# Kernel tuning notes

Measured on AMD Instinct MI355X. Metric: run time of the kernel, lower is better.

The kernel has to match this reference:

```python
import jax, jax.numpy as jnp
import numpy as np
import math

IN_DIM = 256
OUT_DIM = 256
MAX_IN = 1024
MAX_OUT = 512
BATCH = 2
SEQ = 1024  # actual_seq_len == max_in_seq here
RED = 2
LN_EPS = 1e-5


def setup_inputs() -> dict:
    key = jax.random.key(0)
    ks = jax.random.split(key, 8)
    N = BATCH * SEQ
    return {
        "x": jax.random.normal(ks[0], (N, IN_DIM), dtype=jnp.float32),
        "M": jax.random.uniform(ks[1], (OUT_DIM, IN_DIM), minval=-0.5, maxval=0.5, dtype=jnp.float32),
        "P": jax.random.uniform(ks[2], (OUT_DIM, OUT_DIM), minval=-0.1, maxval=0.1, dtype=jnp.float32),
        "Linker": jax.random.uniform(ks[3], (MAX_IN, MAX_OUT), minval=-0.1, maxval=0.1, dtype=jnp.float32),
        "ln_gamma": jnp.ones((OUT_DIM,), dtype=jnp.float32),
        "ln_beta": jnp.zeros((OUT_DIM,), dtype=jnp.float32),
        "res_W": jax.random.uniform(ks[4], (OUT_DIM, IN_DIM), minval=-0.1, maxval=0.1, dtype=jnp.float32),
        "res_linker": jax.random.uniform(ks[5], (MAX_IN, MAX_OUT), minval=-0.1, maxval=0.1, dtype=jnp.float32),
        "actual_seq_len": SEQ,
    }


def _layer_norm(z, gamma, beta):
    mu = jnp.mean(z, axis=-1, keepdims=True)
    var = jnp.mean((z - mu) ** 2, axis=-1, keepdims=True)
    return (z - mu) * jax.lax.rsqrt(var + LN_EPS) * gamma + beta


def _periods():
    i = jnp.arange(OUT_DIM, dtype=jnp.float32)[:, None]
    j = jnp.arange(OUT_DIM, dtype=jnp.float32)[None, :]
    return i * OUT_DIM + j + 2.0  # (D, D)


def reference(x, M, P, Linker, ln_gamma, ln_beta, res_W, res_linker, actual_seq_len):
    S = int(actual_seq_len)
    N, _ = x.shape
    B = N // S
    D = OUT_DIM
    out_seq = max(1, S // RED)

    # Z = LN(x @ M^T)
    Z = _layer_norm(x @ M.T, ln_gamma, ln_beta)  # (N, D)

    # position transform: T[k,i] = sum_j Z[k,j] * P[i,j] * cos(2*pi*k / periods[i,j])
    k = jnp.arange(N, dtype=jnp.float32)[:, None, None]  # (N,1,1)
    phi = jnp.cos(2.0 * math.pi * k / _periods()[None])   # (N, D, D)
    T = jnp.einsum('kj,ij,kij->ki', Z, P, phi)            # (N, D)

    # adaptive sequence-length transform via Linker slice
    L = Linker[:S, :out_seq]                               # (S, out_seq)
    U = jnp.einsum('bsd,st->btd', T.reshape(B, S, D), L).reshape(B * out_seq, D)

    # 'separate' residual path
    rfeat = (x @ res_W.T).reshape(B, S, D)
    rL = res_linker[:S, :out_seq]
    residual = jnp.einsum('bsd,st->btd', rfeat, rL).reshape(B * out_seq, D)

    return U + residual
```

## Files before the change

### kernel.cpp

```cpp
#include <hip/hip_runtime.h>

#define D256 256
#define KT 8
#define S_SEQ 1024
#define OUTSEQ 512

typedef __attribute__((ext_vector_type(8))) short bf16x8;
typedef __attribute__((ext_vector_type(8))) unsigned short u16x8;
typedef __attribute__((ext_vector_type(4))) unsigned short u16x4;
typedef __attribute__((ext_vector_type(4))) float f32x4;

__device__ inline unsigned short f2bf(float f) {
  unsigned u = __float_as_uint(f);
  return (unsigned short)((u + 0x7fffu + ((u >> 16) & 1u)) >> 16);
}

__global__ __launch_bounds__(256) void k_prep(const float* __restrict__ x,
                                              const float* __restrict__ M,
                                              const float* __restrict__ resW,
                                              const float* __restrict__ P,
                                              const float* __restrict__ Linker,
                                              const float* __restrict__ rLinker,
                                              float4* __restrict__ PIt4,
                                              unsigned short* __restrict__ LinkTb,
                                              unsigned short* __restrict__ xb,
                                              unsigned short* __restrict__ Mb,
                                              unsigned short* __restrict__ Wb) {
  __shared__ float tl[64][65];
  const int tid = threadIdx.x;
  const int blk = blockIdx.x;
  if (blk < 256) {
    const int j = blk;
    const int t = tid;
    const float p = (float)(t * D256 + j + 2);
    const float ip = 1.0f / p;
    const float cb2 = 2.0f * __builtin_amdgcn_cosf(ip);
    PIt4[j * D256 + t] = make_float4(P[t * D256 + j], ip, cb2, 0.0f);
    return;
  }
  if (blk >= 512) {
    const float* src;
    unsigned short* dst;
    size_t base;
    if (blk < 768)      { src = x;    dst = xb; base = (size_t)(blk - 512) * 2048; }
    else if (blk < 800) { src = M;    dst = Mb; base = (size_t)(blk - 768) * 2048; }
    else                { src = resW; dst = Wb; base = (size_t)(blk - 800) * 2048; }
    const size_t off = base + (size_t)tid * 8;
    const float4 v0 = *(const float4*)(src + off);
    const float4 v1 = *(const float4*)(src + off + 4);
    u16x8 o;
    o[0] = f2bf(v0.x); o[1] = f2bf(v0.y); o[2] = f2bf(v0.z); o[3] = f2bf(v0.w);
    o[4] = f2bf(v1.x); o[5] = f2bf(v1.y); o[6] = f2bf(v1.z); o[7] = f2bf(v1.w);
    *(u16x8*)(dst + off) = o;
    return;
  }
  const int tb = blk - 256;
  const int st = tb & 31;
  const int tt = tb >> 5;
  const int s0 = st * 64, t0 = tt * 64;
  const float* src = (s0 < 1024) ? (Linker + (size_t)s0 * OUTSEQ)
                                 : (rLinker + (size_t)(s0 - 1024) * OUTSEQ);
  {
    const int sy = tid >> 2, sx = tid & 3;
    #pragma unroll
    for (int c = 0; c < 4; ++c) {
      const int ci = sx + c * 4;
      const float4 v = *(const float4*)&src[sy * OUTSEQ + t0 + ci * 4];
      tl[ci * 4 + 0][sy] = v.x;
      tl[ci * 4 + 1][sy] = v.y;
      tl[ci * 4 + 2][sy] = v.z;
      tl[ci * 4 + 3][sy] = v.w;
    }
  }
  __syncthreads();
  {
    const int ty = tid >> 2, tx = tid & 3;
    u16x8 o0, o1;
    #pragma unroll
    for (int e = 0; e < 8; ++e) o0[e] = f2bf(tl[ty][tx * 16 + e]);
    #pragma unroll
    for (int e = 0; e < 8; ++e) o1[e] = f2bf(tl[ty][tx * 16 + 8 + e]);
    unsigned short* dst = LinkTb + (size_t)(t0 + ty) * 2048 + s0 + tx * 16;
    *(u16x8*)dst = o0;
    *(u16x8*)(dst + 8) = o1;
  }
}

__global__ __launch_bounds__(256) void k_Azn(const unsigned short* __restrict__ xb,
                                             const unsigned short* __restrict__ Mb,
                                             const unsigned short* __restrict__ Wb,
                                             const float* __restrict__ gamma,
                                             const float* __restrict__ beta,
                                             float* __restrict__ Zb,
                                             unsigned short* __restrict__ Bt) {
  __shared__ float Zs[16][D256];
  __shared__ float Rs[16][D256];
  __shared__ float mu_s[16], rs_s[16];
  const int k0 = blockIdx.x * 16;
  const int w = threadIdx.x >> 6;
  const int l = threadIdx.x & 63;
  const int m = l & 15, q = l >> 4;

  f32x4 aZ[4] = {}, aR[4] = {};
  const unsigned short* Arow = xb + (size_t)(k0 + m) * D256;
  #pragma unroll
  for (int ks = 0; ks < 8; ++ks) {
    const bf16x8 a = *(const bf16x8*)(Arow + ks * 32 + q * 8);
    #pragma unroll
    for (int cf = 0; cf < 4; ++cf) {
      const int o = w * 64 + cf * 16 + m;
      const bf16x8 bz = *(const bf16x8*)(Mb + (size_t)o * D256 + ks * 32 + q * 8);
      const bf16x8 br = *(const bf16x8*)(Wb + (size_t)o * D256 + ks * 32 + q * 8);
      aZ[cf] = __builtin_amdgcn_mfma_f32_16x16x32_bf16(a, bz, aZ[cf], 0, 0, 0);
      aR[cf] = __builtin_amdgcn_mfma_f32_16x16x32_bf16(a, br, aR[cf], 0, 0, 0);
    }
  }
  #pragma unroll
  for (int cf = 0; cf < 4; ++cf) {
    #pragma unroll
    for (int r = 0; r < 4; ++r) {
      Zs[q * 4 + r][w * 64 + cf * 16 + m] = aZ[cf][r];
      Rs[q * 4 + r][w * 64 + cf * 16 + m] = aR[cf][r];
    }
  }
  __syncthreads();

  #pragma unroll
  for (int rr = w; rr < 16; rr += 4) {
    float s = 0.f, sq = 0.f;
    #pragma unroll
    for (int p = 0; p < 4; ++p) {
      const float v = Zs[rr][l + 64 * p];
      s += v;
      sq = fmaf(v, v, sq);
    }
    #pragma unroll
    for (int off = 32; off; off >>= 1) {
      s += __shfl_down(s, off);
      sq += __shfl_down(sq, off);
    }
    if (l == 0) {
      const float mu = s * (1.0f / 256.0f);
      const float var = sq * (1.0f / 256.0f) - mu * mu;
      mu_s[rr] = mu;
      rs_s[rr] = rsqrtf(var + 1e-5f);
    }
  }
  __syncthreads();

  {
    const int t = threadIdx.x;
    const float g = gamma[t], be = beta[t];
    u16x8 o0, o1;
    #pragma unroll
    for (int rr = 0; rr < 16; ++rr) {
      Zb[(size_t)(k0 + rr) * D256 + t] = (Zs[rr][t] - mu_s[rr]) * rs_s[rr] * g + be;
      const unsigned short rb = f2bf(Rs[rr][t]);
      if (rr < 8) o0[rr] = rb; else o1[rr - 8] = rb;
    }
    unsigned short* dst = Bt + (size_t)t * 4096 + 2048 + k0;
    *(u16x8*)dst = o0;
    *(u16x8*)(dst + 8) = o1;
  }
}

__global__ __launch_bounds__(256, 6) void k_B(const float* __restrict__ Zb,
                                              const float4* __restrict__ PIt4,
                                              unsigned short* __restrict__ Bt) {
  __shared__ float buf[5120];
  const int tid = threadIdx.x;
  const int il = tid & 7;
  const int jg = tid >> 3;
  const int ig = blockIdx.x & 31;
  const int kt = blockIdx.x >> 5;
  const int i0 = ig * 8;
  const int k0 = kt * 16;
  const int i  = i0 + il;

  #pragma unroll
  for (int r = 0; r < 16; ++r)
    buf[tid * 20 + r] = Zb[(size_t)(k0 + r) * D256 + tid];
  __syncthreads();

  float acc[16] = {};
  const float kf0 = (float)k0;
  const float4* pip = PIt4 + i;
  #pragma unroll
  for (int jj = 0; jj < 8; ++jj) {
    const int j = jg + 32 * jj;
    const float4 pi = pip[(size_t)j * D256];
    const float4 z0 = *(const float4*)&buf[j * 20 + 0];
    const float4 z1 = *(const float4*)&buf[j * 20 + 4];
    const float4 z2 = *(const float4*)&buf[j * 20 + 8];
    const float4 z3 = *(const float4*)&buf[j * 20 + 12];
    const float a = kf0 * pi.y;
    float c0 = __builtin_amdgcn_cosf(__builtin_amdgcn_fractf(a)) * pi.x;
    float c1 = __builtin_amdgcn_cosf(__builtin_amdgcn_fractf(a + pi.y)) * pi.x;
    acc[0] = fmaf(z0.x, c0, acc[0]);
    acc[1] = fmaf(z0.y, c1, acc[1]);
    float c2;
    c2 = fmaf(pi.z, c1, -c0); acc[2]  = fmaf(z0.z, c2, acc[2]);  c0 = c1; c1 = c2;
    c2 = fmaf(pi.z, c1, -c0); acc[3]  = fmaf(z0.w, c2, acc[3]);  c0 = c1; c1 = c2;
    c2 = fmaf(pi.z, c1, -c0); acc[4]  = fmaf(z1.x, c2, acc[4]);  c0 = c1; c1 = c2;
    c2 = fmaf(pi.z, c1, -c0); acc[5]  = fmaf(z1.y, c2, acc[5]);  c0 = c1; c1 = c2;
    c2 = fmaf(pi.z, c1, -c0); acc[6]  = fmaf(z1.z, c2, acc[6]);  c0 = c1; c1 = c2;
    c2 = fmaf(pi.z, c1, -c0); acc[7]  = fmaf(z1.w, c2, acc[7]);  c0 = c1; c1 = c2;
    c2 = fmaf(pi.z, c1, -c0); acc[8]  = fmaf(z2.x, c2, acc[8]);  c0 = c1; c1 = c2;
    c2 = fmaf(pi.z, c1, -c0); acc[9]  = fmaf(z2.y, c2, acc[9]);  c0 = c1; c1 = c2;
    c2 = fmaf(pi.z, c1, -c0); acc[10] = fmaf(z2.z, c2, acc[10]); c0 = c1; c1 = c2;
    c2 = fmaf(pi.z, c1, -c0); acc[11] = fmaf(z2.w, c2, acc[11]); c0 = c1; c1 = c2;
    c2 = fmaf(pi.z, c1, -c0); acc[12] = fmaf(z3.x, c2, acc[12]); c0 = c1; c1 = c2;
    c2 = fmaf(pi.z, c1, -c0); acc[13] = fmaf(z3.y, c2, acc[13]); c0 = c1; c1 = c2;
    c2 = fmaf(pi.z, c1, -c0); acc[14] = fmaf(z3.z, c2, acc[14]); c0 = c1; c1 = c2;
    c2 = fmaf(pi.z, c1, -c0); acc[15] = fmaf(z3.w, c2, acc[15]);
  }
  __syncthreads();

  #pragma unroll
  for (int k = 0; k < 16; ++k)
    buf[jg * 132 + k * 8 + il] = acc[k];
  __syncthreads();

  float tv = 0.f;
  if (tid < 128) {
    #pragma unroll
    for (int g = 0; g < 32; ++g) tv += buf[g * 132 + tid];
  }
  __syncthreads();
  if (tid < 128) buf[(tid & 7) * 16 + (tid >> 3)] = tv;
  __syncthreads();
  if (tid < 32) {
    const int iw = tid >> 2;
    const int kq = tid & 3;
    const float4 v = *(const float4*)&buf[iw * 16 + kq * 4];
    u16x4 o;
    o[0] = f2bf(v.x); o[1] = f2bf(v.y); o[2] = f2bf(v.z); o[3] = f2bf(v.w);
    *(u16x4*)(Bt + (size_t)(i0 + iw) * 4096 + k0 + kq * 4) = o;
  }
}

__global__ __launch_bounds__(256) void k_Cm(const unsigned short* __restrict__ LinkTb,
                                            const unsigned short* __restrict__ Bt,
                                            float* __restrict__ part) {
  const int bid = blockIdx.x;
  const int kc = bid & 7;
  const int dt = (bid >> 3) & 3;
  const int tt = (bid >> 5) & 7;
  const int b  = bid >> 8;
  const int wv = threadIdx.x >> 6;
  const int l  = threadIdx.x & 63;
  const int wm = wv >> 1, wn = wv & 1;
  const int t0 = tt * 64 + wm * 32;
  const int d0 = dt * 64 + wn * 32;
  const int m  = l & 15;
  const int q  = l >> 4;
  const int sc0 = kc * 128;

  f32x4 acc00 = {}, acc01 = {}, acc10 = {}, acc11 = {};
  const unsigned short* Arow = LinkTb + (size_t)(t0 + m) * 2048;
  const unsigned short* Brow = Bt + (size_t)(d0 + m) * 4096;

  #pragma unroll
  for (int seg = 0; seg < 2; ++seg) {
    const int acol = seg * 1024 + sc0 + q * 8;
    const int bcol = seg * 2048 + b * 1024 + sc0 + q * 8;
    #pragma unroll
    for (int ks = 0; ks < 4; ++ks) {
      const bf16x8 a0 = *(const bf16x8*)(Arow + acol + ks * 32);
      const bf16x8 a1 = *(const bf16x8*)(Arow + 16 * 2048 + acol + ks * 32);
      const bf16x8 b0 = *(const bf16x8*)(Brow + bcol + ks * 32);
      const bf16x8 b1 = *(const bf16x8*)(Brow + 16 * 4096 + bcol + ks * 32);
      acc00 = __builtin_amdgcn_mfma_f32_16x16x32_bf16(a0, b0, acc00, 0, 0, 0);
      acc01 = __builtin_amdgcn_mfma_f32_16x16x32_bf16(a0, b1, acc01, 0, 0, 0);
      acc10 = __builtin_amdgcn_mfma_f32_16x16x32_bf16(a1, b0, acc10, 0, 0, 0);
      acc11 = __builtin_amdgcn_mfma_f32_16x16x32_bf16(a1, b1, acc11, 0, 0, 0);
    }
  }

  float* pb = part + ((size_t)kc << 18) + (size_t)(b * 512 + t0 + q * 4) * D256 + d0 + m;
  #pragma unroll
  for (int reg = 0; reg < 4; ++reg) {
    pb[(0 + reg) * D256 + 0]   = acc00[reg];
    pb[(0 + reg) * D256 + 16]  = acc01[reg];
    pb[(16 + reg) * D256 + 0]  = acc10[reg];
    pb[(16 + reg) * D256 + 16] = acc11[reg];
  }
}

__global__ __launch_bounds__(256) void k_Cred(const float* __restrict__ part,
                                              float* __restrict__ out) {
  const int row = blockIdx.x;
  const int d   = threadIdx.x;
  float s = 0.f;
  #pragma unroll
  for (int kc = 0; kc < 8; ++kc)
    s += part[((size_t)kc << 18) + row * D256 + d];
  out[row * D256 + d] = s;
}

extern "C" void kernel_launch(void* const* d_in, const int* in_sizes, int n_in,
                              void* d_out, int out_size, void* d_ws, size_t ws_size,
                              hipStream_t stream) {
  const float* x       = (const float*)d_in[0];
  const float* M       = (const float*)d_in[1];
  const float* P       = (const float*)d_in[2];
  const float* Linker  = (const float*)d_in[3];
  const float* gamma   = (const float*)d_in[4];
  const float* beta    = (const float*)d_in[5];
  const float* resW    = (const float*)d_in[6];
  const float* rLinker = (const float*)d_in[7];
  float* out = (float*)d_out;

  char* ws = (char*)d_ws;
  float4*         PIt4   = (float4*)(ws);
  unsigned short* LinkTb = (unsigned short*)(ws + 1024 * 1024);
  unsigned short* Bt     = (unsigned short*)(ws + 3072 * 1024);
  unsigned short* xb     = (unsigned short*)(ws + 5120 * 1024);
  unsigned short* Mb     = (unsigned short*)(ws + 6144 * 1024);
  unsigned short* Wb     = (unsigned short*)(ws + 6272 * 1024);
  float*          Zb     = (float*)(ws + 6400 * 1024);
  float*          part   = (float*)(ws + 8448 * 1024);

  hipLaunchKernelGGL(k_prep, dim3(832),  dim3(256), 0, stream,
                     x, M, resW, P, Linker, rLinker, PIt4, LinkTb, xb, Mb, Wb);
  hipLaunchKernelGGL(k_Azn,  dim3(128),  dim3(256), 0, stream,
                     xb, Mb, Wb, gamma, beta, Zb, Bt);
  hipLaunchKernelGGL(k_B,    dim3(4096), dim3(256), 0, stream, Zb, PIt4, Bt);
  hipLaunchKernelGGL(k_Cm,   dim3(512),  dim3(256), 0, stream, LinkTb, Bt, part);
  hipLaunchKernelGGL(k_Cred, dim3(1024), dim3(256), 0, stream, part, out);
}
```

Measured before the change: 49.77 us.

## Fuse prep with projection+LayerNorm and reduce split-K partials in shared memory

The first projection GEMM plus LayerNorm now loads fp32 inputs directly and converts them to bf16 in registers. It is merged into the prep kernel, which removes the separate bf16 conversion pass and one launch. The final linker GEMM splits K across the four waves of a block and reduces their partials in LDS. This replaces the global partial buffer and the separate reduction kernel. The change cuts two launches and the partial-sum traffic, at the cost of redundant fp32 loads and conversions of M/resW in each projection block and fewer blocks (256) in the final GEMM.

```diff
diff --git a/kernel.cpp b/kernel.cpp
--- a/kernel.cpp
+++ b/kernel.cpp
@@ -15,22 +15,109 @@
   return (unsigned short)((u + 0x7fffu + ((u >> 16) & 1u)) >> 16);
 }
 
-__global__ __launch_bounds__(256) void k_prep(const float* __restrict__ x,
-                                              const float* __restrict__ M,
-                                              const float* __restrict__ resW,
-                                              const float* __restrict__ P,
-                                              const float* __restrict__ Linker,
-                                              const float* __restrict__ rLinker,
-                                              float4* __restrict__ PIt4,
-                                              unsigned short* __restrict__ LinkTb,
-                                              unsigned short* __restrict__ xb,
-                                              unsigned short* __restrict__ Mb,
-                                              unsigned short* __restrict__ Wb) {
-  __shared__ float tl[64][65];
+__device__ inline bf16x8 ld8bf(const float* p) {
+  const float4 v0 = *(const float4*)p;
+  const float4 v1 = *(const float4*)(p + 4);
+  bf16x8 r;
+  r[0] = (short)f2bf(v0.x); r[1] = (short)f2bf(v0.y);
+  r[2] = (short)f2bf(v0.z); r[3] = (short)f2bf(v0.w);
+  r[4] = (short)f2bf(v1.x); r[5] = (short)f2bf(v1.y);
+  r[6] = (short)f2bf(v1.z); r[7] = (short)f2bf(v1.w);
+  return r;
+}
+
+__global__ __launch_bounds__(256) void k_pre(const float* __restrict__ x,
+                                             const float* __restrict__ M,
+                                             const float* __restrict__ resW,
+                                             const float* __restrict__ P,
+                                             const float* __restrict__ Linker,
+                                             const float* __restrict__ rLinker,
+                                             const float* __restrict__ gamma,
+                                             const float* __restrict__ beta,
+                                             float4* __restrict__ PIt4,
+                                             unsigned short* __restrict__ LinkTb,
+                                             float* __restrict__ Zb,
+                                             unsigned short* __restrict__ Bt) {
+  __shared__ float smem[8224];
   const int tid = threadIdx.x;
   const int blk = blockIdx.x;
-  if (blk < 256) {
-    const int j = blk;
+
+  if (blk < 128) {
+    float (*Zs)[D256] = (float(*)[D256])smem;
+    float (*Rs)[D256] = (float(*)[D256])(smem + 4096);
+    float* mu_s = smem + 8192;
+    float* rs_s = smem + 8208;
+    const int k0 = blk * 16;
+    const int w = tid >> 6;
+    const int l = tid & 63;
+    const int m = l & 15, q = l >> 4;
+
+    f32x4 aZ[4] = {}, aR[4] = {};
+    const float* xrow = x + (size_t)(k0 + m) * D256;
+    #pragma unroll
+    for (int ks = 0; ks < 8; ++ks) {
+      const bf16x8 a = ld8bf(xrow + ks * 32 + q * 8);
+      #pragma unroll
+      for (int cf = 0; cf < 4; ++cf) {
+        const int o = w * 64 + cf * 16 + m;
+        const bf16x8 bz = ld8bf(M    + (size_t)o * D256 + ks * 32 + q * 8);
+        const bf16x8 br = ld8bf(resW + (size_t)o * D256 + ks * 32 + q * 8);
+        aZ[cf] = __builtin_amdgcn_mfma_f32_16x16x32_bf16(a, bz, aZ[cf], 0, 0, 0);
+        aR[cf] = __builtin_amdgcn_mfma_f32_16x16x32_bf16(a, br, aR[cf], 0, 0, 0);
+      }
+    }
+    #pragma unroll
+    for (int cf = 0; cf < 4; ++cf) {
+      #pragma unroll
+      for (int r = 0; r < 4; ++r) {
+        Zs[q * 4 + r][w * 64 + cf * 16 + m] = aZ[cf][r];
+        Rs[q * 4 + r][w * 64 + cf * 16 + m] = aR[cf][r];
+      }
+    }
+    __syncthreads();
+
+    #pragma unroll
+    for (int rr = w; rr < 16; rr += 4) {
+      float s = 0.f, sq = 0.f;
+      #pragma unroll
+      for (int p = 0; p < 4; ++p) {
+        const float v = Zs[rr][l + 64 * p];
+        s += v;
+        sq = fmaf(v, v, sq);
+      }
+      #pragma unroll
+      for (int off = 32; off; off >>= 1) {
+        s += __shfl_down(s, off);
+        sq += __shfl_down(sq, off);
+      }
+      if (l == 0) {
+        const float mu = s * (1.0f / 256.0f);
+        const float var = sq * (1.0f / 256.0f) - mu * mu;
+        mu_s[rr] = mu;
+        rs_s[rr] = rsqrtf(var + 1e-5f);
+      }
+    }
+    __syncthreads();
+
+    {
+      const int t = tid;
+      const float g = gamma[t], be = beta[t];
+      u16x8 o0, o1;
+      #pragma unroll
+      for (int rr = 0; rr < 16; ++rr) {
+        Zb[(size_t)(k0 + rr) * D256 + t] = (Zs[rr][t] - mu_s[rr]) * rs_s[rr] * g + be;
+        const unsigned short rb = f2bf(Rs[rr][t]);
+        if (rr < 8) o0[rr] = rb; else o1[rr - 8] = rb;
+      }
+      unsigned short* dst = Bt + (size_t)t * 4096 + 2048 + k0;
+      *(u16x8*)dst = o0;
+      *(u16x8*)(dst + 8) = o1;
+    }
+    return;
+  }
+
+  if (blk < 384) {
+    const int j = blk - 128;
     const int t = tid;
     const float p = (float)(t * D256 + j + 2);
     const float ip = 1.0f / p;
@@ -38,23 +125,9 @@
     PIt4[j * D256 + t] = make_float4(P[t * D256 + j], ip, cb2, 0.0f);
     return;
   }
-  if (blk >= 512) {
-    const float* src;
-    unsigned short* dst;
-    size_t base;
-    if (blk < 768)      { src = x;    dst = xb; base = (size_t)(blk - 512) * 2048; }
-    else if (blk < 800) { src = M;    dst = Mb; base = (size_t)(blk - 768) * 2048; }
-    else                { src = resW; dst = Wb; base = (size_t)(blk - 800) * 2048; }
-    const size_t off = base + (size_t)tid * 8;
-    const float4 v0 = *(const float4*)(src + off);
-    const float4 v1 = *(const float4*)(src + off + 4);
-    u16x8 o;
-    o[0] = f2bf(v0.x); o[1] = f2bf(v0.y); o[2] = f2bf(v0.z); o[3] = f2bf(v0.w);
-    o[4] = f2bf(v1.x); o[5] = f2bf(v1.y); o[6] = f2bf(v1.z); o[7] = f2bf(v1.w);
-    *(u16x8*)(dst + off) = o;
-    return;
-  }
-  const int tb = blk - 256;
+
+  float (*tl)[65] = (float(*)[65])smem;
+  const int tb = blk - 384;
   const int st = tb & 31;
   const int tt = tb >> 5;
   const int s0 = st * 64, t0 = tt * 64;
@@ -81,84 +154,6 @@
     #pragma unroll
     for (int e = 0; e < 8; ++e) o1[e] = f2bf(tl[ty][tx * 16 + 8 + e]);
     unsigned short* dst = LinkTb + (size_t)(t0 + ty) * 2048 + s0 + tx * 16;
-    *(u16x8*)dst = o0;
-    *(u16x8*)(dst + 8) = o1;
-  }
-}
-
-__global__ __launch_bounds__(256) void k_Azn(const unsigned short* __restrict__ xb,
-                                             const unsigned short* __restrict__ Mb,
-                                             const unsigned short* __restrict__ Wb,
-                                             const float* __restrict__ gamma,
-                                             const float* __restrict__ beta,
-                                             float* __restrict__ Zb,
-                                             unsigned short* __restrict__ Bt) {
-  __shared__ float Zs[16][D256];
-  __shared__ float Rs[16][D256];
-  __shared__ float mu_s[16], rs_s[16];
-  const int k0 = blockIdx.x * 16;
-  const int w = threadIdx.x >> 6;
-  const int l = threadIdx.x & 63;
-  const int m = l & 15, q = l >> 4;
-
-  f32x4 aZ[4] = {}, aR[4] = {};
-  const unsigned short* Arow = xb + (size_t)(k0 + m) * D256;
-  #pragma unroll
-  for (int ks = 0; ks < 8; ++ks) {
-    const bf16x8 a = *(const bf16x8*)(Arow + ks * 32 + q * 8);
-    #pragma unroll
-    for (int cf = 0; cf < 4; ++cf) {
-      const int o = w * 64 + cf * 16 + m;
-      const bf16x8 bz = *(const bf16x8*)(Mb + (size_t)o * D256 + ks * 32 + q * 8);
-      const bf16x8 br = *(const bf16x8*)(Wb + (size_t)o * D256 + ks * 32 + q * 8);
-      aZ[cf] = __builtin_amdgcn_mfma_f32_16x16x32_bf16(a, bz, aZ[cf], 0, 0, 0);
-      aR[cf] = __builtin_amdgcn_mfma_f32_16x16x32_bf16(a, br, aR[cf], 0, 0, 0);
-    }
-  }
-  #pragma unroll
-  for (int cf = 0; cf < 4; ++cf) {
-    #pragma unroll
-    for (int r = 0; r < 4; ++r) {
-      Zs[q * 4 + r][w * 64 + cf * 16 + m] = aZ[cf][r];
-      Rs[q * 4 + r][w * 64 + cf * 16 + m] = aR[cf][r];
-    }
-  }
-  __syncthreads();
-
-  #pragma unroll
-  for (int rr = w; rr < 16; rr += 4) {
-    float s = 0.f, sq = 0.f;
-    #pragma unroll
-    for (int p = 0; p < 4; ++p) {
-      const float v = Zs[rr][l + 64 * p];
-      s += v;
-      sq = fmaf(v, v, sq);
-    }
-    #pragma unroll
-    for (int off = 32; off; off >>= 1) {
-      s += __shfl_down(s, off);
-      sq += __shfl_down(sq, off);
-    }
-    if (l == 0) {
-      const float mu = s * (1.0f / 256.0f);
-      const float var = sq * (1.0f / 256.0f) - mu * mu;
-      mu_s[rr] = mu;
-      rs_s[rr] = rsqrtf(var + 1e-5f);
-    }
-  }
-  __syncthreads();
-
-  {
-    const int t = threadIdx.x;
-    const float g = gamma[t], be = beta[t];
-    u16x8 o0, o1;
-    #pragma unroll
-    for (int rr = 0; rr < 16; ++rr) {
-      Zb[(size_t)(k0 + rr) * D256 + t] = (Zs[rr][t] - mu_s[rr]) * rs_s[rr] * g + be;
-      const unsigned short rb = f2bf(Rs[rr][t]);
-      if (rr < 8) o0[rr] = rb; else o1[rr - 8] = rb;
-    }
-    unsigned short* dst = Bt + (size_t)t * 4096 + 2048 + k0;
     *(u16x8*)dst = o0;
     *(u16x8*)(dst + 8) = o1;
   }
@@ -241,20 +236,18 @@
 
 __global__ __launch_bounds__(256) void k_Cm(const unsigned short* __restrict__ LinkTb,
                                             const unsigned short* __restrict__ Bt,
-                                            float* __restrict__ part) {
+                                            float* __restrict__ out) {
+  __shared__ float red[4][32][32];
   const int bid = blockIdx.x;
-  const int kc = bid & 7;
-  const int dt = (bid >> 3) & 3;
-  const int tt = (bid >> 5) & 7;
-  const int b  = bid >> 8;
-  const int wv = threadIdx.x >> 6;
+  const int ct = bid & 7;
+  const int rt = bid >> 3;
+  const int b  = rt >> 4;
+  const int t0 = (rt & 15) * 32;
+  const int d0 = ct * 32;
+  const int w  = threadIdx.x >> 6;
   const int l  = threadIdx.x & 63;
-  const int wm = wv >> 1, wn = wv & 1;
-  const int t0 = tt * 64 + wm * 32;
-  const int d0 = dt * 64 + wn * 32;
-  const int m  = l & 15;
-  const int q  = l >> 4;
-  const int sc0 = kc * 128;
+  const int m  = l & 15, q = l >> 4;
+  const int s0 = w * 256;
 
   f32x4 acc00 = {}, acc01 = {}, acc10 = {}, acc11 = {};
   const unsigned short* Arow = LinkTb + (size_t)(t0 + m) * 2048;
@@ -262,10 +255,10 @@
 
   #pragma unroll
   for (int seg = 0; seg < 2; ++seg) {
-    const int acol = seg * 1024 + sc0 + q * 8;
-    const int bcol = seg * 2048 + b * 1024 + sc0 + q * 8;
-    #pragma unroll
-    for (int ks = 0; ks < 4; ++ks) {
+    const int acol = seg * 1024 + s0 + q * 8;
+    const int bcol = seg * 2048 + b * 1024 + s0 + q * 8;
+    #pragma unroll
+    for (int ks = 0; ks < 8; ++ks) {
       const bf16x8 a0 = *(const bf16x8*)(Arow + acol + ks * 32);
       const bf16x8 a1 = *(const bf16x8*)(Arow + 16 * 2048 + acol + ks * 32);
       const bf16x8 b0 = *(const bf16x8*)(Brow + bcol + ks * 32);
@@ -277,25 +270,27 @@
     }
   }
 
-  float* pb = part + ((size_t)kc << 18) + (size_t)(b * 512 + t0 + q * 4) * D256 + d0 + m;
-  #pragma unroll
-  for (int reg = 0; reg < 4; ++reg) {
-    pb[(0 + reg) * D256 + 0]   = acc00[reg];
-    pb[(0 + reg) * D256 + 16]  = acc01[reg];
-    pb[(16 + reg) * D256 + 0]  = acc10[reg];
-    pb[(16 + reg) * D256 + 16] = acc11[reg];
-  }
-}
-
-__global__ __launch_bounds__(256) void k_Cred(const float* __restrict__ part,
-                                              float* __restrict__ out) {
-  const int row = blockIdx.x;
-  const int d   = threadIdx.x;
-  float s = 0.f;
-  #pragma unroll
-  for (int kc = 0; kc < 8; ++kc)
-    s += part[((size_t)kc << 18) + row * D256 + d];
-  out[row * D256 + d] = s;
+  #pragma unroll
+  for (int r = 0; r < 4; ++r) {
+    red[w][q * 4 + r][m]           = acc00[r];
+    red[w][q * 4 + r][16 + m]      = acc01[r];
+    red[w][16 + q * 4 + r][m]      = acc10[r];
+    red[w][16 + q * 4 + r][16 + m] = acc11[r];
+  }
+  __syncthreads();
+
+  const int row = threadIdx.x >> 3;
+  const int c4  = (threadIdx.x & 7) * 4;
+  const float4 v0 = *(const float4*)&red[0][row][c4];
+  const float4 v1 = *(const float4*)&red[1][row][c4];
+  const float4 v2 = *(const float4*)&red[2][row][c4];
+  const float4 v3 = *(const float4*)&red[3][row][c4];
+  float4 s;
+  s.x = v0.x + v1.x + v2.x + v3.x;
+  s.y = v0.y + v1.y + v2.y + v3.y;
+  s.z = v0.z + v1.z + v2.z + v3.z;
+  s.w = v0.w + v1.w + v2.w + v3.w;
+  *(float4*)&out[(size_t)(b * 512 + t0 + row) * D256 + d0 + c4] = s;
 }
 
 extern "C" void kernel_launch(void* const* d_in, const int* in_sizes, int n_in,
@@ -315,17 +310,11 @@
   float4*         PIt4   = (float4*)(ws);
   unsigned short* LinkTb = (unsigned short*)(ws + 1024 * 1024);
   unsigned short* Bt     = (unsigned short*)(ws + 3072 * 1024);
-  unsigned short* xb     = (unsigned short*)(ws + 5120 * 1024);
-  unsigned short* Mb     = (unsigned short*)(ws + 6144 * 1024);
-  unsigned short* Wb     = (unsigned short*)(ws + 6272 * 1024);
-  float*          Zb     = (float*)(ws + 6400 * 1024);
-  float*          part   = (float*)(ws + 8448 * 1024);
-
-  hipLaunchKernelGGL(k_prep, dim3(832),  dim3(256), 0, stream,
-                     x, M, resW, P, Linker, rLinker, PIt4, LinkTb, xb, Mb, Wb);
-  hipLaunchKernelGGL(k_Azn,  dim3(128),  dim3(256), 0, stream,
-                     xb, Mb, Wb, gamma, beta, Zb, Bt);
-  hipLaunchKernelGGL(k_B,    dim3(4096), dim3(256), 0, stream, Zb, PIt4, Bt);
-  hipLaunchKernelGGL(k_Cm,   dim3(512),  dim3(256), 0, stream, LinkTb, Bt, part);
-  hipLaunchKernelGGL(k_Cred, dim3(1024), dim3(256), 0, stream, part, out);
-}
+  float*          Zb     = (float*)(ws + 5120 * 1024);
+
+  hipLaunchKernelGGL(k_pre, dim3(640),  dim3(256), 0, stream,
+                     x, M, resW, P, Linker, rLinker, gamma, beta,
+                     PIt4, LinkTb, Zb, Bt);
+  hipLaunchKernelGGL(k_B,   dim3(4096), dim3(256), 0, stream, Zb, PIt4, Bt);
+  hipLaunchKernelGGL(k_Cm,  dim3(256),  dim3(256), 0, stream, LinkTb, Bt, out);
+}
```

Result: slower. 51.07 us (+2.6%).

## Restructure position-transform kernel with stride-2 packed cosine recurrence and transposed Z

Applied to the files above, without the earlier changes.

The LN output Z is now written transposed (feature-major), so k_B can read each feature's 32 consecutive sequence values straight from global memory instead of staging them in LDS. k_B now covers 32 positions per block and steps the Chebyshev cosine recurrence by two. It uses a precomputed 4cos²θ−2 coefficient and packed f32x2 FMAs, which roughly halves the FMA instruction count. The cross-thread reduction is simplified to a single LDS pass with scalar bf16 stores. The trade-offs are more register pressure (occupancy hint lowered from 6 to 4), a larger LDS buffer, and uncoalesced 2-byte output stores.

```diff
diff --git a/kernel.cpp b/kernel.cpp
--- a/kernel.cpp
+++ b/kernel.cpp
@@ -1,14 +1,13 @@
 #include <hip/hip_runtime.h>
 
 #define D256 256
-#define KT 8
 #define S_SEQ 1024
 #define OUTSEQ 512
 
 typedef __attribute__((ext_vector_type(8))) short bf16x8;
 typedef __attribute__((ext_vector_type(8))) unsigned short u16x8;
-typedef __attribute__((ext_vector_type(4))) unsigned short u16x4;
 typedef __attribute__((ext_vector_type(4))) float f32x4;
+typedef __attribute__((ext_vector_type(2))) float f32x2;
 
 __device__ inline unsigned short f2bf(float f) {
   unsigned u = __float_as_uint(f);
@@ -35,7 +34,8 @@
     const float p = (float)(t * D256 + j + 2);
     const float ip = 1.0f / p;
     const float cb2 = 2.0f * __builtin_amdgcn_cosf(ip);
-    PIt4[j * D256 + t] = make_float4(P[t * D256 + j], ip, cb2, 0.0f);
+    const float D = fmaf(cb2, cb2, -2.0f);
+    PIt4[j * D256 + t] = make_float4(P[t * D256 + j], ip, cb2, D);
     return;
   }
   if (blk >= 512) {
@@ -91,7 +91,7 @@
                                              const unsigned short* __restrict__ Wb,
                                              const float* __restrict__ gamma,
                                              const float* __restrict__ beta,
-                                             float* __restrict__ Zb,
+                                             float* __restrict__ ZbT,
                                              unsigned short* __restrict__ Bt) {
   __shared__ float Zs[16][D256];
   __shared__ float Rs[16][D256];
@@ -151,92 +151,102 @@
   {
     const int t = threadIdx.x;
     const float g = gamma[t], be = beta[t];
+    float zt[16];
     u16x8 o0, o1;
     #pragma unroll
     for (int rr = 0; rr < 16; ++rr) {
-      Zb[(size_t)(k0 + rr) * D256 + t] = (Zs[rr][t] - mu_s[rr]) * rs_s[rr] * g + be;
+      zt[rr] = (Zs[rr][t] - mu_s[rr]) * rs_s[rr] * g + be;
       const unsigned short rb = f2bf(Rs[rr][t]);
       if (rr < 8) o0[rr] = rb; else o1[rr - 8] = rb;
     }
+    float* zd = ZbT + (size_t)t * 2048 + k0;
+    *(float4*)(zd + 0)  = make_float4(zt[0], zt[1], zt[2], zt[3]);
+    *(float4*)(zd + 4)  = make_float4(zt[4], zt[5], zt[6], zt[7]);
+    *(float4*)(zd + 8)  = make_float4(zt[8], zt[9], zt[10], zt[11]);
+    *(float4*)(zd + 12) = make_float4(zt[12], zt[13], zt[14], zt[15]);
     unsigned short* dst = Bt + (size_t)t * 4096 + 2048 + k0;
     *(u16x8*)dst = o0;
     *(u16x8*)(dst + 8) = o1;
   }
 }
 
-__global__ __launch_bounds__(256, 6) void k_B(const float* __restrict__ Zb,
+__global__ __launch_bounds__(256, 4) void k_B(const float* __restrict__ ZbT,
                                               const float4* __restrict__ PIt4,
                                               unsigned short* __restrict__ Bt) {
-  __shared__ float buf[5120];
+  __shared__ float buf[8448];
   const int tid = threadIdx.x;
   const int il = tid & 7;
   const int jg = tid >> 3;
   const int ig = blockIdx.x & 31;
   const int kt = blockIdx.x >> 5;
   const int i0 = ig * 8;
-  const int k0 = kt * 16;
+  const int k0 = kt * 32;
   const int i  = i0 + il;
 
-  #pragma unroll
-  for (int r = 0; r < 16; ++r)
-    buf[tid * 20 + r] = Zb[(size_t)(k0 + r) * D256 + tid];
+  f32x2 acc[16];
+  #pragma unroll
+  for (int q = 0; q < 16; ++q) acc[q] = (f32x2){0.f, 0.f};
+
+  const float kf0 = (float)k0;
+  #pragma unroll
+  for (int jj = 0; jj < 8; ++jj) {
+    const int j = jg * 8 + jj;
+    const f32x4 pi = *(const f32x4*)&PIt4[(size_t)j * D256 + i];
+    const float* zr = ZbT + (size_t)j * 2048 + k0;
+    const f32x4 z0 = *(const f32x4*)(zr + 0);
+    const f32x4 z1 = *(const f32x4*)(zr + 4);
+    const f32x4 z2 = *(const f32x4*)(zr + 8);
+    const f32x4 z3 = *(const f32x4*)(zr + 12);
+    const f32x4 z4 = *(const f32x4*)(zr + 16);
+    const f32x4 z5 = *(const f32x4*)(zr + 20);
+    const f32x4 z6 = *(const f32x4*)(zr + 24);
+    const f32x4 z7 = *(const f32x4*)(zr + 28);
+    const float a  = kf0 * pi.y;
+    const float r0 = __builtin_amdgcn_fractf(a);
+    const float r1 = __builtin_amdgcn_fractf(a + pi.y);
+    const float s0 = __builtin_amdgcn_cosf(r0) * pi.x;
+    const float s1 = __builtin_amdgcn_cosf(r1) * pi.x;
+    const float s2 = fmaf(pi.z, s1, -s0);
+    const float s3 = fmaf(pi.z, s2, -s1);
+    f32x2 pm1 = {s0, s1};
+    f32x2 pm  = {s2, s3};
+    const f32x2 D2 = {pi.w, pi.w};
+    acc[0] = __builtin_elementwise_fma((f32x2){z0.x, z0.y}, pm1, acc[0]);
+    acc[1] = __builtin_elementwise_fma((f32x2){z0.z, z0.w}, pm,  acc[1]);
+    f32x2 pn;
+#define CSTEP(IDX, ZA, ZB) \
+    pn = __builtin_elementwise_fma(D2, pm, -pm1); \
+    acc[IDX] = __builtin_elementwise_fma((f32x2){ZA, ZB}, pn, acc[IDX]); \
+    pm1 = pm; pm = pn;
+    CSTEP(2,  z1.x, z1.y)
+    CSTEP(3,  z1.z, z1.w)
+    CSTEP(4,  z2.x, z2.y)
+    CSTEP(5,  z2.z, z2.w)
+    CSTEP(6,  z3.x, z3.y)
+    CSTEP(7,  z3.z, z3.w)
+    CSTEP(8,  z4.x, z4.y)
+    CSTEP(9,  z4.z, z4.w)
+    CSTEP(10, z5.x, z5.y)
+    CSTEP(11, z5.z, z5.w)
+    CSTEP(12, z6.x, z6.y)
+    CSTEP(13, z6.z, z6.w)
+    CSTEP(14, z7.x, z7.y)
+    CSTEP(15, z7.z, z7.w)
+#undef CSTEP
+  }
+
+  #pragma unroll
+  for (int k2 = 0; k2 < 16; ++k2) {
+    buf[jg * 264 + il * 33 + k2 * 2]     = acc[k2].x;
+    buf[jg * 264 + il * 33 + k2 * 2 + 1] = acc[k2].y;
+  }
   __syncthreads();
 
-  float acc[16] = {};
-  const float kf0 = (float)k0;
-  const float4* pip = PIt4 + i;
-  #pragma unroll
-  for (int jj = 0; jj < 8; ++jj) {
-    const int j = jg + 32 * jj;
-    const float4 pi = pip[(size_t)j * D256];
-    const float4 z0 = *(const float4*)&buf[j * 20 + 0];
-    const float4 z1 = *(const float4*)&buf[j * 20 + 4];
-    const float4 z2 = *(const float4*)&buf[j * 20 + 8];
-    const float4 z3 = *(const float4*)&buf[j * 20 + 12];
-    const float a = kf0 * pi.y;
-    float c0 = __builtin_amdgcn_cosf(__builtin_amdgcn_fractf(a)) * pi.x;
-    float c1 = __builtin_amdgcn_cosf(__builtin_amdgcn_fractf(a + pi.y)) * pi.x;
-    acc[0] = fmaf(z0.x, c0, acc[0]);
-    acc[1] = fmaf(z0.y, c1, acc[1]);
-    float c2;
-    c2 = fmaf(pi.z, c1, -c0); acc[2]  = fmaf(z0.z, c2, acc[2]);  c0 = c1; c1 = c2;
-    c2 = fmaf(pi.z, c1, -c0); acc[3]  = fmaf(z0.w, c2, acc[3]);  c0 = c1; c1 = c2;
-    c2 = fmaf(pi.z, c1, -c0); acc[4]  = fmaf(z1.x, c2, acc[4]);  c0 = c1; c1 = c2;
-    c2 = fmaf(pi.z, c1, -c0); acc[5]  = fmaf(z1.y, c2, acc[5]);  c0 = c1; c1 = c2;
-    c2 = fmaf(pi.z, c1, -c0); acc[6]  = fmaf(z1.z, c2, acc[6]);  c0 = c1; c1 = c2;
-    c2 = fmaf(pi.z, c1, -c0); acc[7]  = fmaf(z1.w, c2, acc[7]);  c0 = c1; c1 = c2;
-    c2 = fmaf(pi.z, c1, -c0); acc[8]  = fmaf(z2.x, c2, acc[8]);  c0 = c1; c1 = c2;
-    c2 = fmaf(pi.z, c1, -c0); acc[9]  = fmaf(z2.y, c2, acc[9]);  c0 = c1; c1 = c2;
-    c2 = fmaf(pi.z, c1, -c0); acc[10] = fmaf(z2.z, c2, acc[10]); c0 = c1; c1 = c2;
-    c2 = fmaf(pi.z, c1, -c0); acc[11] = fmaf(z2.w, c2, acc[11]); c0 = c1; c1 = c2;
-    c2 = fmaf(pi.z, c1, -c0); acc[12] = fmaf(z3.x, c2, acc[12]); c0 = c1; c1 = c2;
-    c2 = fmaf(pi.z, c1, -c0); acc[13] = fmaf(z3.y, c2, acc[13]); c0 = c1; c1 = c2;
-    c2 = fmaf(pi.z, c1, -c0); acc[14] = fmaf(z3.z, c2, acc[14]); c0 = c1; c1 = c2;
-    c2 = fmaf(pi.z, c1, -c0); acc[15] = fmaf(z3.w, c2, acc[15]);
-  }
-  __syncthreads();
-
-  #pragma unroll
-  for (int k = 0; k < 16; ++k)
-    buf[jg * 132 + k * 8 + il] = acc[k];
-  __syncthreads();
-
+  const int ir = tid >> 5, kr = tid & 31;
   float tv = 0.f;
-  if (tid < 128) {
-    #pragma unroll
-    for (int g = 0; g < 32; ++g) tv += buf[g * 132 + tid];
-  }
-  __syncthreads();
-  if (tid < 128) buf[(tid & 7) * 16 + (tid >> 3)] = tv;
-  __syncthreads();
-  if (tid < 32) {
-    const int iw = tid >> 2;
-    const int kq = tid & 3;
-    const float4 v = *(const float4*)&buf[iw * 16 + kq * 4];
-    u16x4 o;
-    o[0] = f2bf(v.x); o[1] = f2bf(v.y); o[2] = f2bf(v.z); o[3] = f2bf(v.w);
-    *(u16x4*)(Bt + (size_t)(i0 + iw) * 4096 + k0 + kq * 4) = o;
-  }
+  #pragma unroll
+  for (int g = 0; g < 32; ++g) tv += buf[g * 264 + ir * 33 + kr];
+  Bt[(size_t)(i0 + ir) * 4096 + k0 + kr] = f2bf(tv);
 }
 
 __global__ __launch_bounds__(256) void k_Cm(const unsigned short* __restrict__ LinkTb,
@@ -318,14 +328,14 @@
   unsigned short* xb     = (unsigned short*)(ws + 5120 * 1024);
   unsigned short* Mb     = (unsigned short*)(ws + 6144 * 1024);
   unsigned short* Wb     = (unsigned short*)(ws + 6272 * 1024);
-  float*          Zb     = (float*)(ws + 6400 * 1024);
+  float*          ZbT    = (float*)(ws + 6400 * 1024);
   float*          part   = (float*)(ws + 8448 * 1024);
 
   hipLaunchKernelGGL(k_prep, dim3(832),  dim3(256), 0, stream,
                      x, M, resW, P, Linker, rLinker, PIt4, LinkTb, xb, Mb, Wb);
   hipLaunchKernelGGL(k_Azn,  dim3(128),  dim3(256), 0, stream,
-                     xb, Mb, Wb, gamma, beta, Zb, Bt);
-  hipLaunchKernelGGL(k_B,    dim3(4096), dim3(256), 0, stream, Zb, PIt4, Bt);
+                     xb, Mb, Wb, gamma, beta, ZbT, Bt);
+  hipLaunchKernelGGL(k_B,    dim3(2048), dim3(256), 0, stream, ZbT, PIt4, Bt);
   hipLaunchKernelGGL(k_Cm,   dim3(512),  dim3(256), 0, stream, LinkTb, Bt, part);
   hipLaunchKernelGGL(k_Cred, dim3(1024), dim3(256), 0, stream, part, out);
 }
```

After: 56.11 us. 1.13x slower.
